# Optimization experiments

Measured on AMD Instinct MI355X. Metric: run time of the kernel, lower is better.

The kernel has to match this reference:

```python
import jax, jax.numpy as jnp
import numpy as np

EPS = 1e-12


def _cosine_cost_volume(ref, tgt, D):
    """PSMNet-style shifted cosine-correlation cost volume, num_groups=1.
    ref, tgt: [B, C, Hf, Wf] quarter-res features. Returns [B, 1, D, Hf, Wf];
    positions w < d are 0 (zero-padded target -> zero cosine)."""
    B, C, Hf, Wf = ref.shape
    rn = ref * jax.lax.rsqrt(jnp.sum(ref * ref, axis=1, keepdims=True) + EPS)
    tn = tgt * jax.lax.rsqrt(jnp.sum(tgt * tgt, axis=1, keepdims=True) + EPS)
    pad = jnp.pad(tn, ((0, 0), (0, 0), (0, 0), (D - 1, 0)))  # left zero-pad

    def one_disp(d):
        t = jax.lax.dynamic_slice_in_dim(pad, D - 1 - d, Wf, axis=3)
        return jnp.sum(rn * t, axis=1)  # [B, Hf, Wf]

    vol = jax.vmap(one_disp)(jnp.arange(D))  # [D, B, Hf, Wf]
    return jnp.transpose(vol, (1, 0, 2, 3))[:, None]  # [B, 1, D, Hf, Wf]


def setup_inputs() -> dict:
    key = jax.random.key(0)
    k1, k2 = jax.random.split(key)
    B, C, Hf, Wf = 1, 32, 96, 192  # quarter-res ViT features (out_feats=32)
    left_fea = jax.random.normal(k1, (B, C, Hf, Wf), dtype=jnp.float32)
    right_fea = jax.random.normal(k2, (B, C, Hf, Wf), dtype=jnp.float32)
    return {"left_fea": left_fea, "right_fea": right_fea, "H": 384, "W": 768, "maxdisp": 192}


def reference(left_fea, right_fea, H, W, maxdisp):
    B = left_fea.shape[0]
    # training-branch cost volume (W//4 disparity levels, not detached in source)
    cost_init = _cosine_cost_volume(left_fea, right_fea, W // 4)
    # inference path: maxdisp//4 levels, trilinear upsample to [maxdisp, H, W]
    cost = _cosine_cost_volume(left_fea, right_fea, maxdisp // 4)
    cost = jax.lax.stop_gradient(cost)
    cost_up = jax.image.resize(cost, (B, 1, maxdisp, H, W), method="trilinear")
    pred = jnp.argmax(cost_up, axis=2)  # [B, 1, H, W]
    pred = jnp.maximum(pred, 1).astype(jnp.float32)  # pred[pred<1]=1
    return cost_init, pred
```

## Files before the change

### kernel.cpp

```cpp
#include <hip/hip_runtime.h>
#include <math.h>

#define HF 96
#define WF 192
#define CC 32
#define NPIX (HF*WF)
#define DFULL 192
#define DQ 48
#define HO 384
#define WO 768

__global__ __launch_bounds__(192) void kcost(const float* __restrict__ L,
                                             const float* __restrict__ R,
                                             float* __restrict__ out) {
    __shared__ float rs[CC * WF];
    const int h = blockIdx.x;
    const int y = blockIdx.y;
    const int w = threadIdx.x;

    {
        float rreg[CC];
        float s = 0.0f;
        #pragma unroll
        for (int c = 0; c < CC; ++c) {
            float v = R[c * NPIX + h * WF + w];
            rreg[c] = v;
            s = fmaf(v, v, s);
        }
        float rinv = 1.0f / sqrtf(s + 1e-12f);
        #pragma unroll
        for (int c = 0; c < CC; ++c)
            rs[c * WF + w] = rreg[c] * rinv;
    }

    float lreg[CC];
    {
        float s = 0.0f;
        #pragma unroll
        for (int c = 0; c < CC; ++c) {
            float v = L[c * NPIX + h * WF + w];
            lreg[c] = v;
            s = fmaf(v, v, s);
        }
        float linv = 1.0f / sqrtf(s + 1e-12f);
        #pragma unroll
        for (int c = 0; c < CC; ++c) lreg[c] *= linv;
    }

    __syncthreads();

    for (int dd = 0; dd < 48; ++dd) {
        int d = 4 * dd + y;
        int wp = w - d;
        float acc = 0.0f;
        if (wp >= 0) {
            #pragma unroll
            for (int c = 0; c < CC; ++c)
                acc = fmaf(lreg[c], rs[c * WF + wp], acc);
        }
        out[(d * HF + h) * WF + w] = acc;
    }
}

__global__ __launch_bounds__(256) void kpred(const float* __restrict__ cost,
                                             float* __restrict__ pred) {
    int pid = blockIdx.x * 256 + threadIdx.x;
    if (pid >= HO * WO) return;
    int w = pid % WO;
    int h = pid / WO;

    float sh = (float)(2 * h - 3) * 0.125f;
    float fh = sh - floorf(sh);
    int h0 = (int)floorf(sh);
    int h1 = h0 + 1;
    if (h0 < 0)      { h0 = 0; h1 = 0; fh = 0.0f; }
    if (h1 > HF - 1) { h1 = HF - 1;    fh = 0.0f; }

    float sw = (float)(2 * w - 3) * 0.125f;
    float fw = sw - floorf(sw);
    int w0 = (int)floorf(sw);
    int w1 = w0 + 1;
    if (w0 < 0)      { w0 = 0; w1 = 0; fw = 0.0f; }
    if (w1 > WF - 1) { w1 = WF - 1;    fw = 0.0f; }

    const float wh0 = 1.0f - fh, wh1 = fh;
    const float ww0 = 1.0f - fw, ww1 = fw;

    const int i00 = h0 * WF + w0;
    const int i10 = h1 * WF + w0;
    const int i01 = h0 * WF + w1;
    const int i11 = h1 * WF + w1;

    auto bilin = [&](int k) -> float {
        const float* s = cost + k * NPIX;
        float v00 = s[i00], v10 = s[i10], v01 = s[i01], v11 = s[i11];
        float a0 = fmaf(wh1, v10, wh0 * v00);
        float a1 = fmaf(wh1, v11, wh0 * v01);
        return fmaf(ww1, a1, ww0 * a0);
    };

    float bprev = bilin(0);
    float best = bprev;
    int bidx = 0;

    for (int k = 1; k < DQ; ++k) {
        float b = bilin(k);
        #pragma unroll
        for (int t = 0; t < 4; ++t) {
            float f = 0.125f + 0.25f * (float)t;
            float v = fmaf(f, b, (1.0f - f) * bprev);
            if (v > best) { best = v; bidx = 4 * k - 2 + t; }
        }
        bprev = b;
    }
    if (bprev > best) { best = bprev; bidx = 190; }

    pred[pid] = (float)(bidx < 1 ? 1 : bidx);
}

extern "C" void kernel_launch(void* const* d_in, const int* in_sizes, int n_in,
                              void* d_out, int out_size, void* d_ws, size_t ws_size,
                              hipStream_t stream) {
    const float* L = (const float*)d_in[0];
    const float* R = (const float*)d_in[1];
    float* out = (float*)d_out;
    float* pred = out + DFULL * NPIX;

    kcost<<<dim3(HF, 4), 192, 0, stream>>>(L, R, out);
    kpred<<<(HO * WO + 255) / 256, 256, 0, stream>>>(out, pred);
}
```

Measured before the change: 102.6 us.

## Register-tile cost volume over triangular tiles and share bilinear work in argmax

The cost kernel now normalizes both feature rows into shared memory and assigns each thread a 4x4 (width x disparity) tile over the valid triangle. Each thread accumulates with float4 LDS loads and writes float4 stores, with separate zero-fill of the invalid upper triangle. The prediction kernel has each thread handle one quarter-res column interval, computing the bilinear-in-height blend once and deriving four output pixels. It also uses a monotone-segment shortcut to test only one candidate per disparity interval and writes float2 outputs. This cuts redundant LDS reads and FLOPs and avoids launching work for zero regions, at the cost of complex index mapping, and the argmax shortcut could alter tie-breaking.

Result: faster. 99.02 us (-3.5%).

```diff
diff --git a/kernel.cpp b/kernel.cpp
--- a/kernel.cpp
+++ b/kernel.cpp
@@ -9,65 +9,102 @@
 #define DQ 48
 #define HO 384
 #define WO 768
+#define SR 200
 
-__global__ __launch_bounds__(192) void kcost(const float* __restrict__ L,
+__global__ __launch_bounds__(256) void kcost(const float* __restrict__ L,
                                              const float* __restrict__ R,
                                              float* __restrict__ out) {
-    __shared__ float rs[CC * WF];
+    __shared__ __align__(16) float Ls[CC * WF];
+    __shared__ __align__(16) float Rb[CC * SR];
     const int h = blockIdx.x;
-    const int y = blockIdx.y;
-    const int w = threadIdx.x;
+    const int tid = threadIdx.x;
+
+    for (int i = tid; i < CC * 4; i += 256) Rb[(i >> 2) * SR + (i & 3)] = 0.0f;
+
+    if (tid < WF) {
+        const int w = tid;
+        float lr[CC], rr[CC];
+        float sl = 0.0f, sr = 0.0f;
+        #pragma unroll
+        for (int c = 0; c < CC; ++c) {
+            float lv = L[c * NPIX + h * WF + w];
+            float rv = R[c * NPIX + h * WF + w];
+            lr[c] = lv; rr[c] = rv;
+            sl = fmaf(lv, lv, sl);
+            sr = fmaf(rv, rv, sr);
+        }
+        const float il = 1.0f / sqrtf(sl + 1e-12f);
+        const float ir = 1.0f / sqrtf(sr + 1e-12f);
+        #pragma unroll
+        for (int c = 0; c < CC; ++c) {
+            Ls[c * WF + w] = lr[c] * il;
+            Rb[c * SR + 4 + w] = rr[c] * ir;
+        }
+    }
+    __syncthreads();
+
+    const int t = blockIdx.y * 256 + tid;
+    if (t >= 1176) return;
+
+    const int u = 1175 - t;
+    int wu = (int)((sqrtf(8.0f * (float)u + 1.0f) - 1.0f) * 0.5f);
+    while ((wu + 1) * (wu + 2) / 2 <= u) ++wu;
+    while (wu * (wu + 1) / 2 > u) --wu;
+    const int du = u - wu * (wu + 1) / 2;
+    const int wt = 47 - du;
+    const int dt = 47 - wu;
+
+    const int w0 = wt * 4, d0 = dt * 4;
+    const int base = w0 - d0;
+
+    float a00=0,a01=0,a02=0,a03=0;
+    float a10=0,a11=0,a12=0,a13=0;
+    float a20=0,a21=0,a22=0,a23=0;
+    float a30=0,a31=0,a32=0,a33=0;
+
+    #pragma unroll 4
+    for (int c = 0; c < CC; ++c) {
+        const float4 lv = *(const float4*)&Ls[c * WF + w0];
+        const float4 r0 = *(const float4*)&Rb[c * SR + base];
+        const float4 r1 = *(const float4*)&Rb[c * SR + base + 4];
+        a00 = fmaf(lv.x, r1.x, a00); a01 = fmaf(lv.y, r1.y, a01);
+        a02 = fmaf(lv.z, r1.z, a02); a03 = fmaf(lv.w, r1.w, a03);
+        a10 = fmaf(lv.x, r0.w, a10); a11 = fmaf(lv.y, r1.x, a11);
+        a12 = fmaf(lv.z, r1.y, a12); a13 = fmaf(lv.w, r1.z, a13);
+        a20 = fmaf(lv.x, r0.z, a20); a21 = fmaf(lv.y, r0.w, a21);
+        a22 = fmaf(lv.z, r1.x, a22); a23 = fmaf(lv.w, r1.y, a23);
+        a30 = fmaf(lv.x, r0.y, a30); a31 = fmaf(lv.y, r0.z, a31);
+        a32 = fmaf(lv.z, r0.w, a32); a33 = fmaf(lv.w, r1.x, a33);
+    }
 
     {
-        float rreg[CC];
-        float s = 0.0f;
-        #pragma unroll
-        for (int c = 0; c < CC; ++c) {
-            float v = R[c * NPIX + h * WF + w];
-            rreg[c] = v;
-            s = fmaf(v, v, s);
-        }
-        float rinv = 1.0f / sqrtf(s + 1e-12f);
-        #pragma unroll
-        for (int c = 0; c < CC; ++c)
-            rs[c * WF + w] = rreg[c] * rinv;
+        float4 v;
+        v.x=a00; v.y=a01; v.z=a02; v.w=a03;
+        *(float4*)&out[(d0 + 0) * NPIX + h * WF + w0] = v;
+        v.x=a10; v.y=a11; v.z=a12; v.w=a13;
+        *(float4*)&out[(d0 + 1) * NPIX + h * WF + w0] = v;
+        v.x=a20; v.y=a21; v.z=a22; v.w=a23;
+        *(float4*)&out[(d0 + 2) * NPIX + h * WF + w0] = v;
+        v.x=a30; v.y=a31; v.z=a32; v.w=a33;
+        *(float4*)&out[(d0 + 3) * NPIX + h * WF + w0] = v;
     }
 
-    float lreg[CC];
-    {
-        float s = 0.0f;
+    if (wt > dt) {
+        const int za = (wt - dt - 1) * 4;
+        const int zb = (47 - dt) * 4;
+        const float4 z = {0.0f, 0.0f, 0.0f, 0.0f};
         #pragma unroll
-        for (int c = 0; c < CC; ++c) {
-            float v = L[c * NPIX + h * WF + w];
-            lreg[c] = v;
-            s = fmaf(v, v, s);
-        }
-        float linv = 1.0f / sqrtf(s + 1e-12f);
-        #pragma unroll
-        for (int c = 0; c < CC; ++c) lreg[c] *= linv;
-    }
-
-    __syncthreads();
-
-    for (int dd = 0; dd < 48; ++dd) {
-        int d = 4 * dd + y;
-        int wp = w - d;
-        float acc = 0.0f;
-        if (wp >= 0) {
-            #pragma unroll
-            for (int c = 0; c < CC; ++c)
-                acc = fmaf(lreg[c], rs[c * WF + wp], acc);
-        }
-        out[(d * HF + h) * WF + w] = acc;
+        for (int j = 0; j < 4; ++j)
+            *(float4*)&out[(zb + j) * NPIX + h * WF + za] = z;
     }
 }
 
 __global__ __launch_bounds__(256) void kpred(const float* __restrict__ cost,
                                              float* __restrict__ pred) {
-    int pid = blockIdx.x * 256 + threadIdx.x;
-    if (pid >= HO * WO) return;
-    int w = pid % WO;
-    int h = pid / WO;
+    const int mIdx = blockIdx.x * 64 + threadIdx.x;
+    const int h = blockIdx.y * 4 + threadIdx.y;
+    if (mIdx > 192) return;
+    const int m = mIdx - 1;
 
     float sh = (float)(2 * h - 3) * 0.125f;
     float fh = sh - floorf(sh);
@@ -75,47 +112,72 @@
     int h1 = h0 + 1;
     if (h0 < 0)      { h0 = 0; h1 = 0; fh = 0.0f; }
     if (h1 > HF - 1) { h1 = HF - 1;    fh = 0.0f; }
+    const float wh0 = 1.0f - fh, wh1 = fh;
 
-    float sw = (float)(2 * w - 3) * 0.125f;
-    float fw = sw - floorf(sw);
-    int w0 = (int)floorf(sw);
-    int w1 = w0 + 1;
-    if (w0 < 0)      { w0 = 0; w1 = 0; fw = 0.0f; }
-    if (w1 > WF - 1) { w1 = WF - 1;    fw = 0.0f; }
+    const bool edge = (m < 0) || (m >= WF - 1);
+    const int w0 = (m < 0) ? 0 : ((m >= WF - 1) ? WF - 1 : m);
+    const int w1 = (m < 0) ? 0 : ((m >= WF - 1) ? WF - 1 : m + 1);
 
-    const float wh0 = 1.0f - fh, wh1 = fh;
-    const float ww0 = 1.0f - fw, ww1 = fw;
+    float fr[4];
+    #pragma unroll
+    for (int r = 0; r < 4; ++r) fr[r] = edge ? 0.0f : (0.125f + 0.25f * (float)r);
 
     const int i00 = h0 * WF + w0;
     const int i10 = h1 * WF + w0;
     const int i01 = h0 * WF + w1;
     const int i11 = h1 * WF + w1;
 
-    auto bilin = [&](int k) -> float {
-        const float* s = cost + k * NPIX;
-        float v00 = s[i00], v10 = s[i10], v01 = s[i01], v11 = s[i11];
-        float a0 = fmaf(wh1, v10, wh0 * v00);
-        float a1 = fmaf(wh1, v11, wh0 * v01);
-        return fmaf(ww1, a1, ww0 * a0);
-    };
-
-    float bprev = bilin(0);
-    float best = bprev;
-    int bidx = 0;
+    float bp[4], best[4];
+    int bi[4];
+    {
+        const float* s = cost;
+        float q00 = s[i00], q10 = s[i10], q01 = s[i01], q11 = s[i11];
+        float A0 = fmaf(wh1, q10, wh0 * q00);
+        float A1 = fmaf(wh1, q11, wh0 * q01);
+        #pragma unroll
+        for (int r = 0; r < 4; ++r) {
+            bp[r] = fmaf(fr[r], A1, (1.0f - fr[r]) * A0);
+            best[r] = bp[r];
+            bi[r] = 0;
+        }
+    }
 
     for (int k = 1; k < DQ; ++k) {
-        float b = bilin(k);
+        const float* s = cost + k * NPIX;
+        float q00 = s[i00], q10 = s[i10], q01 = s[i01], q11 = s[i11];
+        float A0 = fmaf(wh1, q10, wh0 * q00);
+        float A1 = fmaf(wh1, q11, wh0 * q01);
         #pragma unroll
-        for (int t = 0; t < 4; ++t) {
-            float f = 0.125f + 0.25f * (float)t;
-            float v = fmaf(f, b, (1.0f - f) * bprev);
-            if (v > best) { best = v; bidx = 4 * k - 2 + t; }
+        for (int r = 0; r < 4; ++r) {
+            float b = fmaf(fr[r], A1, (1.0f - fr[r]) * A0);
+            float cand; int ci;
+            if (b > bp[r]) { cand = fmaf(0.875f, b, 0.125f * bp[r]); ci = 4 * k + 1; }
+            else           { cand = fmaf(0.125f, b, 0.875f * bp[r]); ci = 4 * k - 2; }
+            if (cand > best[r]) { best[r] = cand; bi[r] = ci; }
+            bp[r] = b;
         }
-        bprev = b;
     }
-    if (bprev > best) { best = bprev; bidx = 190; }
+    #pragma unroll
+    for (int r = 0; r < 4; ++r)
+        if (bp[r] > best[r]) bi[r] = 190;
 
-    pred[pid] = (float)(bidx < 1 ? 1 : bidx);
+    float v[4];
+    #pragma unroll
+    for (int r = 0; r < 4; ++r) v[r] = (float)(bi[r] < 1 ? 1 : bi[r]);
+
+    float* prow = pred + h * WO;
+    if (m < 0) {
+        float2 o; o.x = v[0]; o.y = v[0];
+        *(float2*)&prow[0] = o;
+    } else if (m >= WF - 1) {
+        float2 o; o.x = v[0]; o.y = v[0];
+        *(float2*)&prow[WO - 2] = o;
+    } else {
+        float2 o0; o0.x = v[0]; o0.y = v[1];
+        float2 o1; o1.x = v[2]; o1.y = v[3];
+        *(float2*)&prow[4 * m + 2] = o0;
+        *(float2*)&prow[4 * m + 4] = o1;
+    }
 }
 
 extern "C" void kernel_launch(void* const* d_in, const int* in_sizes, int n_in,
@@ -126,6 +188,6 @@
     float* out = (float*)d_out;
     float* pred = out + DFULL * NPIX;
 
-    kcost<<<dim3(HF, 4), 192, 0, stream>>>(L, R, out);
-    kpred<<<(HO * WO + 255) / 256, 256, 0, stream>>>(out, pred);
+    kcost<<<dim3(HF, 5), 256, 0, stream>>>(L, R, out);
+    kpred<<<dim3(4, HF), dim3(64, 4), 0, stream>>>(out, pred);
 }
```
